# Performance work log

Measured on AMD Instinct MI355X. Metric: run time of the kernel, lower is better.

The kernel has to match this reference:

```python
import jax, jax.numpy as jnp
import numpy as np

N_NODES = 100000
N_EDGES = 600000
N_GRAPHS = 512
F_IN = 128
F_HID = 128
F_OUT = 128


def setup_inputs() -> dict:
    key = jax.random.key(0)
    ks = jax.random.split(key, 10)
    x = jax.random.normal(ks[0], (N_NODES, F_IN), dtype=jnp.float32)
    edge_index = jax.random.randint(ks[1], (2, N_EDGES), 0, N_NODES, dtype=jnp.int64)
    batch = jnp.sort(jax.random.randint(ks[2], (N_NODES,), 0, N_GRAPHS, dtype=jnp.int64))
    s1 = 1.0 / np.sqrt(F_IN)
    s2 = 1.0 / np.sqrt(F_HID)
    s3 = 1.0 / np.sqrt(F_OUT)
    W1 = jax.random.uniform(ks[3], (F_IN, F_HID), jnp.float32, -s1, s1)
    b1 = jnp.zeros((F_HID,), jnp.float32)
    W2 = jax.random.uniform(ks[4], (F_HID, F_OUT), jnp.float32, -s2, s2)
    b2 = jnp.zeros((F_OUT,), jnp.float32)
    Wlin = jax.random.uniform(ks[5], (F_OUT, 1), jnp.float32, -s3, s3)
    blin = jax.random.uniform(ks[6], (1,), jnp.float32, -s3, s3)
    return {"x": x, "edge_index": edge_index, "batch": batch,
            "W1": W1, "b1": b1, "W2": W2, "b2": b2, "Wlin": Wlin, "blin": blin}


def reference(x, edge_index, batch, W1, b1, W2, b2, Wlin, blin):
    N = x.shape[0]
    # GCN normalization with self-loops: D^{-1/2} (A + I) D^{-1/2}
    loop = jnp.arange(N, dtype=edge_index.dtype)
    src = jnp.concatenate([edge_index[0], loop])  # [E + N]
    dst = jnp.concatenate([edge_index[1], loop])
    deg = jax.ops.segment_sum(jnp.ones_like(dst, dtype=x.dtype), dst, num_segments=N)
    dis = jnp.where(deg > 0, jax.lax.rsqrt(jnp.maximum(deg, 1.0)), 0.0)  # deg^{-1/2}
    norm = (dis[src] * dis[dst])[:, None]  # [E+N, 1] edge weights

    def gcn_conv(h, W, b):
        hW = h @ W                                      # [N, d_out]
        msgs = norm * hW[src]                           # gather + scale
        agg = jax.ops.segment_sum(msgs, dst, num_segments=N)  # scatter-add
        return agg + b

    h = jax.nn.relu(gcn_conv(x, W1, b1))
    h = gcn_conv(h, W2, b2)

    # global_mean_pool over graph ids
    counts = jax.ops.segment_sum(jnp.ones((N,), x.dtype), batch, num_segments=N_GRAPHS)
    pooled = jax.ops.segment_sum(h, batch, num_segments=N_GRAPHS)
    pooled = pooled / jnp.maximum(counts, 1.0)[:, None]  # [N_GRAPHS, F_OUT]

    # dropout is identity in eval mode
    return pooled @ Wlin + blin  # [N_GRAPHS, 1]
```

## Files before the change

### kernel.cpp

```cpp
#include <hip/hip_runtime.h>

#define F 128

typedef __bf16 bf16x8 __attribute__((ext_vector_type(8)));
typedef float f32x4 __attribute__((ext_vector_type(4)));

__global__ __launch_bounds__(256) void k_prep(const float* __restrict__ W1, const float* __restrict__ W2,
                                              const float* __restrict__ Wlin, const float* __restrict__ b2,
                                              const float* __restrict__ blin, const int* __restrict__ batch,
                                              __bf16* __restrict__ Bswz, float* __restrict__ w2l,
                                              float* __restrict__ cconst, int* __restrict__ gstart,
                                              int* __restrict__ histg, float* __restrict__ deg,
                                              int N, int G, int bG) {
    int bid = blockIdx.x;
    int tid = threadIdx.x;
    if (bid < 64) {
        int o = bid * 256 + tid;
        int j = o & 7, lane = (o >> 3) & 63, tc = o >> 9;
        int t = tc >> 3, c = tc & 7;
        int k = t * 32 + (lane >> 4) * 8 + j;
        int n = c * 16 + (lane & 15);
        Bswz[o] = (__bf16)W1[k * F + n];
    } else if (bid == 64) {
        __shared__ float sh[F];
        if (tid < F) {
            float s = 0.0f;
            for (int j = 0; j < F; j += 4) {
                float4 w = *(const float4*)&W2[tid * F + j];
                float4 l = *(const float4*)&Wlin[j];
                s += w.x * l.x + w.y * l.y + w.z * l.z + w.w * l.w;
            }
            w2l[tid] = s;
            sh[tid] = b2[tid] * Wlin[tid];
        } else if (tid < F + 64) {
            histg[tid - F] = 0;
        }
        __syncthreads();
        if (tid == 0) {
            float c = blin[0];
            for (int j = 0; j < F; ++j) c += sh[j];
            *cconst = c;
        }
    } else if (bid < 65 + bG) {
        int g = (bid - 65) * 256 + tid;
        if (g < G) {
            int lo = 0, hi = N;
            while (lo < hi) { int mid = (lo + hi) >> 1; if (batch[mid] < g) lo = mid + 1; else hi = mid; }
            gstart[g] = lo;
            if (g == 0) gstart[G] = N;
        }
    } else {
        int i = (bid - 65 - bG) * 256 + tid;
        if (i < N) deg[i] = 1.0f;
    }
}

__global__ __launch_bounds__(256) void k_count(const int* __restrict__ dst, float* deg, int E) {
    int base = (blockIdx.x * 256 + threadIdx.x) * 4;
    if (base + 4 <= E) {
        int4 d = *(const int4*)(dst + base);
        unsafeAtomicAdd(&deg[d.x], 1.0f);
        unsafeAtomicAdd(&deg[d.y], 1.0f);
        unsafeAtomicAdd(&deg[d.z], 1.0f);
        unsafeAtomicAdd(&deg[d.w], 1.0f);
    } else {
        for (int i = base; i < E; ++i) unsafeAtomicAdd(&deg[dst[i]], 1.0f);
    }
}

__global__ __launch_bounds__(256) void k_scan1(const float* __restrict__ deg, int* __restrict__ pref,
                                               int* __restrict__ bsum, float* __restrict__ dis,
                                               int* __restrict__ histg, int N) {
    int t = threadIdx.x;
    __shared__ int lh[64];
    __shared__ int wtot[4];
    if (t < 64) lh[t] = 0;
    int base = blockIdx.x * 1024 + t * 4;
    int v[4]; int s = 0;
#pragma unroll
    for (int j = 0; j < 4; ++j) {
        int idx = base + j;
        float dv = (idx < N) ? deg[idx] : 1.0f;
        if (idx < N) dis[idx] = rsqrtf(dv);
        v[j] = (idx < N) ? ((int)dv - 1) : 0; s += v[j];
    }
    int lane = t & 63, w = t >> 6;
    int inc = s;
#pragma unroll
    for (int d = 1; d < 64; d <<= 1) { int o = __shfl_up(inc, d); if (lane >= d) inc += o; }
    if (lane == 63) wtot[w] = inc;
    __syncthreads();
#pragma unroll
    for (int j = 0; j < 4; ++j)
        if (base + j < N) atomicAdd(&lh[min(v[j], 63)], 1);
    int woff = 0;
#pragma unroll
    for (int i = 0; i < 4; ++i) if (i < w) woff += wtot[i];
    int run = woff + inc - s;
#pragma unroll
    for (int j = 0; j < 4; ++j) { int idx = base + j; if (idx < N) pref[idx] = run; run += v[j]; }
    if (t == 255) bsum[blockIdx.x] = woff + inc;
    __syncthreads();
    if (t < 64 && lh[t] > 0) atomicAdd(&histg[t], lh[t]);
}

__global__ __launch_bounds__(256) void k_scan3(int* __restrict__ pref, const int* __restrict__ bsum,
                                               int* __restrict__ cursor, const int* __restrict__ histg,
                                               int* __restrict__ bcur, int N, int E) {
    int t = threadIdx.x;
    int chunk = blockIdx.x >> 2;
    int partial = 0;
    for (int i = t; i < chunk; i += 256) partial += bsum[i];
    int lane = t & 63, w = t >> 6;
#pragma unroll
    for (int d = 1; d < 64; d <<= 1) partial += __shfl_xor(partial, d);
    __shared__ int ws4[4];
    if (lane == 0) ws4[w] = partial;
    __syncthreads();
    int off = ws4[0] + ws4[1] + ws4[2] + ws4[3];
    int i = blockIdx.x * 256 + t;
    if (i < N) {
        int v = pref[i] + off;
        pref[i] = v;
        cursor[i] = v;
    }
    if (i == 0) pref[N] = E;
    if (blockIdx.x == 0 && t < 64) {
        int h = histg[t];
        int inc2 = h;
#pragma unroll
        for (int d = 1; d < 64; d <<= 1) { int o = __shfl_up(inc2, d); if (t >= d) inc2 += o; }
        bcur[t] = inc2 - h;
    }
}

__global__ __launch_bounds__(256) void k_fill(const int* __restrict__ src, const int* __restrict__ dst,
                                              const float* __restrict__ deg, int* __restrict__ cursor,
                                              int* __restrict__ srcs, int* __restrict__ bcur,
                                              int* __restrict__ perm, int E, int N, int nbN) {
    int bid = blockIdx.x, tid = threadIdx.x;
    if (bid < nbN) {
        __shared__ int lcnt[64], lbase[64];
        if (tid < 64) lcnt[tid] = 0;
        __syncthreads();
        int n = bid * 256 + tid;
        int b = 0, r = 0;
        if (n < N) {
            b = min((int)deg[n] - 1, 63);
            r = atomicAdd(&lcnt[b], 1);
        }
        __syncthreads();
        if (tid < 64 && lcnt[tid] > 0) lbase[tid] = atomicAdd(&bcur[tid], lcnt[tid]);
        __syncthreads();
        if (n < N) perm[lbase[b] + r] = n;
    } else {
        int base = ((bid - nbN) * 256 + tid) * 4;
        if (base + 4 <= E) {
            int4 s4 = *(const int4*)(src + base);
            int4 d4 = *(const int4*)(dst + base);
            srcs[atomicAdd(&cursor[d4.x], 1)] = s4.x;
            srcs[atomicAdd(&cursor[d4.y], 1)] = s4.y;
            srcs[atomicAdd(&cursor[d4.z], 1)] = s4.z;
            srcs[atomicAdd(&cursor[d4.w], 1)] = s4.w;
        } else {
            for (int e = base; e < E; ++e) {
                srcs[atomicAdd(&cursor[dst[e]], 1)] = src[e];
            }
        }
    }
}

__global__ __launch_bounds__(256) void k_gemm_mfma(const float* __restrict__ X,
                                                   const __bf16* __restrict__ Bswz,
                                                   const float* __restrict__ dis,
                                                   __bf16* __restrict__ Yb, int N) {
    int lane = threadIdx.x & 63, wave = threadIdx.x >> 6;
    int quad = lane >> 4, m = lane & 15;
    int r0 = blockIdx.x * 128 + wave * 32;

    f32x4 acc[2][8];
#pragma unroll
    for (int rt = 0; rt < 2; ++rt)
#pragma unroll
        for (int c = 0; c < 8; ++c) acc[rt][c] = (f32x4)0.0f;

    int ra = r0 + m;      if (ra >= N) ra = N - 1;
    int rb = r0 + 16 + m; if (rb >= N) rb = N - 1;
    const float* pxa = &X[(size_t)ra * F + quad * 8];
    const float* pxb = &X[(size_t)rb * F + quad * 8];

    float4 a0 = *(const float4*)pxa, a1 = *(const float4*)(pxa + 4);
    float4 a2 = *(const float4*)pxb, a3 = *(const float4*)(pxb + 4);

#pragma unroll 1
    for (int t = 0; t < 4; ++t) {
        const __bf16* bp = Bswz + (size_t)t * 4096 + lane * 8;
        bf16x8 B[8];
#pragma unroll
        for (int c = 0; c < 8; ++c) B[c] = *(const bf16x8*)(bp + c * 512);

        float fa[8] = {a0.x, a0.y, a0.z, a0.w, a1.x, a1.y, a1.z, a1.w};
        float fb[8] = {a2.x, a2.y, a2.z, a2.w, a3.x, a3.y, a3.z, a3.w};
        bf16x8 ah0, al0, ah1, al1;
#pragma unroll
        for (int j = 0; j < 8; ++j) {
            __bf16 h0 = (__bf16)fa[j]; ah0[j] = h0; al0[j] = (__bf16)(fa[j] - (float)h0);
            __bf16 h1 = (__bf16)fb[j]; ah1[j] = h1; al1[j] = (__bf16)(fb[j] - (float)h1);
        }
        if (t < 3) {
            a0 = *(const float4*)(pxa + (t + 1) * 32);
            a1 = *(const float4*)(pxa + (t + 1) * 32 + 4);
            a2 = *(const float4*)(pxb + (t + 1) * 32);
            a3 = *(const float4*)(pxb + (t + 1) * 32 + 4);
        }
#pragma unroll
        for (int c = 0; c < 8; ++c) {
            acc[0][c] = __builtin_amdgcn_mfma_f32_16x16x32_bf16(ah0, B[c], acc[0][c], 0, 0, 0);
            acc[0][c] = __builtin_amdgcn_mfma_f32_16x16x32_bf16(al0, B[c], acc[0][c], 0, 0, 0);
            acc[1][c] = __builtin_amdgcn_mfma_f32_16x16x32_bf16(ah1, B[c], acc[1][c], 0, 0, 0);
            acc[1][c] = __builtin_amdgcn_mfma_f32_16x16x32_bf16(al1, B[c], acc[1][c], 0, 0, 0);
        }
    }

#pragma unroll
    for (int rt = 0; rt < 2; ++rt) {
        int rbase = r0 + rt * 16 + quad * 4;
#pragma unroll
        for (int r = 0; r < 4; ++r) {
            int row = rbase + r;
            if (row < N) {
                float dr = dis[row];
#pragma unroll
                for (int c = 0; c < 8; ++c)
                    Yb[(size_t)row * F + c * 16 + m] = (__bf16)(acc[rt][c][r] * dr);
            }
        }
    }
}

__global__ __launch_bounds__(256) void k_agg_z(const __bf16* __restrict__ hWb, const float* __restrict__ dis,
                                               const int* __restrict__ rowptr, const int* __restrict__ srcs,
                                               const int* __restrict__ perm,
                                               const float* __restrict__ bias, const float* __restrict__ w2l,
                                               float* __restrict__ zt, int N) {
    int idx = blockIdx.x * 32 + (threadIdx.x >> 3);
    if (idx >= N) return;
    int node = perm[idx];
    int lane = threadIdx.x & 7;
    float di = dis[node];
    float s[16];
    {
        const __bf16* pr = &hWb[(size_t)node * F + lane * 16];
        bf16x8 v0 = *(const bf16x8*)pr;
        bf16x8 v1 = *(const bf16x8*)(pr + 8);
#pragma unroll
        for (int j = 0; j < 8; ++j) { s[j] = (float)v0[j]; s[8 + j] = (float)v1[j]; }
    }
    int e0 = rowptr[node], e1 = rowptr[node + 1];
    int e = e0;
    for (; e + 4 <= e1; e += 4) {
        int i0 = srcs[e], i1 = srcs[e + 1], i2 = srcs[e + 2], i3 = srcs[e + 3];
        const __bf16* p0 = &hWb[(size_t)i0 * F + lane * 16];
        const __bf16* p1 = &hWb[(size_t)i1 * F + lane * 16];
        const __bf16* p2 = &hWb[(size_t)i2 * F + lane * 16];
        const __bf16* p3 = &hWb[(size_t)i3 * F + lane * 16];
        bf16x8 a0 = *(const bf16x8*)p0, b0 = *(const bf16x8*)(p0 + 8);
        bf16x8 a1 = *(const bf16x8*)p1, b1 = *(const bf16x8*)(p1 + 8);
        bf16x8 a2 = *(const bf16x8*)p2, b2 = *(const bf16x8*)(p2 + 8);
        bf16x8 a3 = *(const bf16x8*)p3, b3 = *(const bf16x8*)(p3 + 8);
#pragma unroll
        for (int j = 0; j < 8; ++j) {
            s[j]     += (float)a0[j] + (float)a1[j] + (float)a2[j] + (float)a3[j];
            s[8 + j] += (float)b0[j] + (float)b1[j] + (float)b2[j] + (float)b3[j];
        }
    }
    for (; e < e1; ++e) {
        const __bf16* pr = &hWb[(size_t)srcs[e] * F + lane * 16];
        bf16x8 v0 = *(const bf16x8*)pr;
        bf16x8 v1 = *(const bf16x8*)(pr + 8);
#pragma unroll
        for (int j = 0; j < 8; ++j) { s[j] += (float)v0[j]; s[8 + j] += (float)v1[j]; }
    }
    float p = 0.0f;
#pragma unroll
    for (int q = 0; q < 4; ++q) {
        float4 bb = *(const float4*)&bias[lane * 16 + q * 4];
        float4 ww = *(const float4*)&w2l[lane * 16 + q * 4];
        p += fmaxf(fmaf(di, s[q * 4 + 0], bb.x), 0.0f) * ww.x;
        p += fmaxf(fmaf(di, s[q * 4 + 1], bb.y), 0.0f) * ww.y;
        p += fmaxf(fmaf(di, s[q * 4 + 2], bb.z), 0.0f) * ww.z;
        p += fmaxf(fmaf(di, s[q * 4 + 3], bb.w), 0.0f) * ww.w;
    }
#pragma unroll
    for (int d = 1; d < 8; d <<= 1) p += __shfl_xor(p, d);
    if (lane == 0) zt[node] = di * p;
}

__global__ __launch_bounds__(256) void k_pool(const float* __restrict__ zt, const float* __restrict__ dis,
                                              const int* __restrict__ rowptr, const int* __restrict__ srcs,
                                              const int* __restrict__ gstart, const float* __restrict__ cconst,
                                              const float* __restrict__ blin, float* __restrict__ out, int G) {
    int g = blockIdx.x;
    int g0 = gstart[g], g1 = gstart[g + 1];
    float acc = 0.0f;
    for (int n = g0 + threadIdx.x; n < g1; n += 256) {
        float s = zt[n];
        int e0 = rowptr[n], e1 = rowptr[n + 1];
        int e = e0;
        for (; e + 4 <= e1; e += 4) {
            s += zt[srcs[e]] + zt[srcs[e + 1]] + zt[srcs[e + 2]] + zt[srcs[e + 3]];
        }
        for (; e < e1; ++e) s += zt[srcs[e]];
        acc += dis[n] * s;
    }
#pragma unroll
    for (int d = 1; d < 64; d <<= 1) acc += __shfl_xor(acc, d);
    __shared__ float ws4[4];
    if ((threadIdx.x & 63) == 0) ws4[threadIdx.x >> 6] = acc;
    __syncthreads();
    if (threadIdx.x == 0) {
        float sum = ws4[0] + ws4[1] + ws4[2] + ws4[3];
        int c = g1 - g0;
        out[g] = (c > 0) ? (sum / (float)c + cconst[0]) : blin[0];
    }
}


extern "C" void kernel_launch(void* const* d_in, const int* in_sizes, int n_in,
                              void* d_out, int out_size, void* d_ws, size_t ws_size,
                              hipStream_t stream) {
    const float* x    = (const float*)d_in[0];
    const int*   ei   = (const int*)d_in[1];
    const int*   batch= (const int*)d_in[2];
    const float* W1   = (const float*)d_in[3];
    const float* b1   = (const float*)d_in[4];
    const float* W2   = (const float*)d_in[5];
    const float* b2   = (const float*)d_in[6];
    const float* Wlin = (const float*)d_in[7];
    const float* blin = (const float*)d_in[8];
    float* out = (float*)d_out;

    const int N = in_sizes[2];
    const int E = in_sizes[1] / 2;
    const int G = out_size;
    const int* src = ei;
    const int* dst = ei + E;

    char* p = (char*)d_ws;
    auto take = [&](size_t bytes) { char* q = p; p += (bytes + 255) & ~(size_t)255; return q; };
    __bf16* hWb    = (__bf16*)take((size_t)N * F * 2);
    float*  ztbuf  = (float*)take((size_t)N * 4);
    float*  deg    = (float*)take((size_t)N * 4);
    float*  dis    = (float*)take((size_t)N * 4);
    int*    rowptr = (int*)  take((size_t)(N + 1) * 4);
    int*    cursor = (int*)  take((size_t)N * 4);
    int*    srcs   = (int*)  take((size_t)E * 4);
    int*    perm   = (int*)  take((size_t)N * 4);
    int*    bsum   = (int*)  take(4096);
    int*    histg  = (int*)  take(64 * 4);
    int*    bcur   = (int*)  take(64 * 4);
    int*    gstart = (int*)  take((size_t)(G + 1) * 4);
    float*  w2l    = (float*)take((size_t)F * 4);
    float*  cconst = (float*)take(256);
    __bf16* Bswz   = (__bf16*)take((size_t)F * F * 2);

    const int nbN  = (N + 255) / 256;
    const int nbE4 = (E + 1023) / 1024;
    const int nbS  = (N + 1023) / 1024;
    const int bG   = (G + 255) / 256;

    k_prep <<<65 + bG + nbN, 256, 0, stream>>>(W1, W2, Wlin, b2, blin, batch,
                                               Bswz, w2l, cconst, gstart, histg, deg, N, G, bG);
    k_count<<<nbE4, 256, 0, stream>>>(dst, deg, E);
    k_scan1<<<nbS, 256, 0, stream>>>(deg, rowptr, bsum, dis, histg, N);
    k_scan3<<<nbN, 256, 0, stream>>>(rowptr, bsum, cursor, histg, bcur, N, E);
    k_fill <<<nbN + nbE4, 256, 0, stream>>>(src, dst, deg, cursor, srcs, bcur, perm, E, N, nbN);

    k_gemm_mfma<<<(N + 127) / 128, 256, 0, stream>>>(x, Bswz, dis, hWb, N);
    k_agg_z<<<(N + 31) / 32, 256, 0, stream>>>(hWb, dis, rowptr, srcs, perm, b1, w2l, ztbuf, N);
    k_pool <<<G, 256, 0, stream>>>(ztbuf, dis, rowptr, srcs, gstart, cconst, blin, out, G);
}
```

Baseline: 222.8 us.

## Fuse CSR build into one cooperative kernel and parallelize pooling per node

Merges the degree count, two scan passes and CSR fill kernels into a single cooperative launch of persistent blocks separated by grid-wide syncs, which removes several kernel launch gaps. Pooling moves from one block per graph to one thread per degree-sorted node, adding each node's value into per-graph accumulators with atomics, followed by a small finalize kernel. The cooperative launch requires 1024 blocks to be co-resident, and grid syncs plus float atomics make the summation order nondeterministic.

```diff
diff --git a/kernel.cpp b/kernel.cpp
--- a/kernel.cpp
+++ b/kernel.cpp
@@ -1,4 +1,7 @@
 #include <hip/hip_runtime.h>
+#include <hip/hip_cooperative_groups.h>
+
+namespace cg = cooperative_groups;
 
 #define F 128
 
@@ -11,7 +14,7 @@
                                               __bf16* __restrict__ Bswz, float* __restrict__ w2l,
                                               float* __restrict__ cconst, int* __restrict__ gstart,
                                               int* __restrict__ histg, float* __restrict__ deg,
-                                              int N, int G, int bG) {
+                                              float* __restrict__ gacc, int N, int G, int bG) {
     int bid = blockIdx.x;
     int tid = threadIdx.x;
     if (bid < 64) {
@@ -47,6 +50,7 @@
             int lo = 0, hi = N;
             while (lo < hi) { int mid = (lo + hi) >> 1; if (batch[mid] < g) lo = mid + 1; else hi = mid; }
             gstart[g] = lo;
+            gacc[g] = 0.0f;
             if (g == 0) gstart[G] = N;
         }
     } else {
@@ -55,95 +59,96 @@
     }
 }
 
-__global__ __launch_bounds__(256) void k_count(const int* __restrict__ dst, float* deg, int E) {
-    int base = (blockIdx.x * 256 + threadIdx.x) * 4;
-    if (base + 4 <= E) {
-        int4 d = *(const int4*)(dst + base);
+__global__ __launch_bounds__(256, 4) void k_graph(const int* __restrict__ src, const int* __restrict__ dst,
+                                                  float* __restrict__ deg, int* __restrict__ pref,
+                                                  int* __restrict__ bsum, float* __restrict__ dis,
+                                                  int* __restrict__ histg, int* __restrict__ cursor,
+                                                  int* __restrict__ srcs, int* __restrict__ bcur,
+                                                  int* __restrict__ perm,
+                                                  int N, int E, int nbN, int nbS) {
+    cg::grid_group grid = cg::this_grid();
+    int tid = threadIdx.x;
+    int nthreads = gridDim.x * 256;
+    __shared__ int lh[64];
+    __shared__ int wtot[4];
+    __shared__ int ws4[4];
+    __shared__ int lcnt[64], lbase[64];
+
+    for (int i = blockIdx.x * 256 + tid; i < (E >> 2); i += nthreads) {
+        int4 d = *(const int4*)(dst + i * 4);
         unsafeAtomicAdd(&deg[d.x], 1.0f);
         unsafeAtomicAdd(&deg[d.y], 1.0f);
         unsafeAtomicAdd(&deg[d.z], 1.0f);
         unsafeAtomicAdd(&deg[d.w], 1.0f);
-    } else {
-        for (int i = base; i < E; ++i) unsafeAtomicAdd(&deg[dst[i]], 1.0f);
-    }
-}
-
-__global__ __launch_bounds__(256) void k_scan1(const float* __restrict__ deg, int* __restrict__ pref,
-                                               int* __restrict__ bsum, float* __restrict__ dis,
-                                               int* __restrict__ histg, int N) {
-    int t = threadIdx.x;
-    __shared__ int lh[64];
-    __shared__ int wtot[4];
-    if (t < 64) lh[t] = 0;
-    int base = blockIdx.x * 1024 + t * 4;
-    int v[4]; int s = 0;
-#pragma unroll
-    for (int j = 0; j < 4; ++j) {
-        int idx = base + j;
-        float dv = (idx < N) ? deg[idx] : 1.0f;
-        if (idx < N) dis[idx] = rsqrtf(dv);
-        v[j] = (idx < N) ? ((int)dv - 1) : 0; s += v[j];
-    }
-    int lane = t & 63, w = t >> 6;
-    int inc = s;
-#pragma unroll
-    for (int d = 1; d < 64; d <<= 1) { int o = __shfl_up(inc, d); if (lane >= d) inc += o; }
-    if (lane == 63) wtot[w] = inc;
-    __syncthreads();
-#pragma unroll
-    for (int j = 0; j < 4; ++j)
-        if (base + j < N) atomicAdd(&lh[min(v[j], 63)], 1);
-    int woff = 0;
-#pragma unroll
-    for (int i = 0; i < 4; ++i) if (i < w) woff += wtot[i];
-    int run = woff + inc - s;
-#pragma unroll
-    for (int j = 0; j < 4; ++j) { int idx = base + j; if (idx < N) pref[idx] = run; run += v[j]; }
-    if (t == 255) bsum[blockIdx.x] = woff + inc;
-    __syncthreads();
-    if (t < 64 && lh[t] > 0) atomicAdd(&histg[t], lh[t]);
-}
-
-__global__ __launch_bounds__(256) void k_scan3(int* __restrict__ pref, const int* __restrict__ bsum,
-                                               int* __restrict__ cursor, const int* __restrict__ histg,
-                                               int* __restrict__ bcur, int N, int E) {
-    int t = threadIdx.x;
-    int chunk = blockIdx.x >> 2;
-    int partial = 0;
-    for (int i = t; i < chunk; i += 256) partial += bsum[i];
-    int lane = t & 63, w = t >> 6;
-#pragma unroll
-    for (int d = 1; d < 64; d <<= 1) partial += __shfl_xor(partial, d);
-    __shared__ int ws4[4];
-    if (lane == 0) ws4[w] = partial;
-    __syncthreads();
-    int off = ws4[0] + ws4[1] + ws4[2] + ws4[3];
-    int i = blockIdx.x * 256 + t;
-    if (i < N) {
-        int v = pref[i] + off;
-        pref[i] = v;
-        cursor[i] = v;
-    }
-    if (i == 0) pref[N] = E;
-    if (blockIdx.x == 0 && t < 64) {
-        int h = histg[t];
+    }
+    if (blockIdx.x == 0 && tid < (E & 3))
+        unsafeAtomicAdd(&deg[dst[(E & ~3) + tid]], 1.0f);
+    grid.sync();
+
+    for (int vb = blockIdx.x; vb < nbS; vb += gridDim.x) {
+        if (tid < 64) lh[tid] = 0;
+        int base = vb * 1024 + tid * 4;
+        int v[4]; int s = 0;
+#pragma unroll
+        for (int j = 0; j < 4; ++j) {
+            int idx = base + j;
+            float dv = (idx < N) ? deg[idx] : 1.0f;
+            if (idx < N) dis[idx] = rsqrtf(dv);
+            v[j] = (idx < N) ? ((int)dv - 1) : 0; s += v[j];
+        }
+        int lane = tid & 63, w = tid >> 6;
+        int inc = s;
+#pragma unroll
+        for (int d = 1; d < 64; d <<= 1) { int o = __shfl_up(inc, d); if (lane >= d) inc += o; }
+        if (lane == 63) wtot[w] = inc;
+        __syncthreads();
+#pragma unroll
+        for (int j = 0; j < 4; ++j)
+            if (base + j < N) atomicAdd(&lh[min(v[j], 63)], 1);
+        int woff = 0;
+#pragma unroll
+        for (int i = 0; i < 4; ++i) if (i < w) woff += wtot[i];
+        int run = woff + inc - s;
+#pragma unroll
+        for (int j = 0; j < 4; ++j) { int idx = base + j; if (idx < N) pref[idx] = run; run += v[j]; }
+        if (tid == 255) bsum[vb] = woff + inc;
+        __syncthreads();
+        if (tid < 64 && lh[tid] > 0) atomicAdd(&histg[tid], lh[tid]);
+    }
+    grid.sync();
+
+    for (int vb = blockIdx.x; vb < nbN; vb += gridDim.x) {
+        int chunk = vb >> 2;
+        int partial = 0;
+        for (int i = tid; i < chunk; i += 256) partial += bsum[i];
+        int lane = tid & 63, w = tid >> 6;
+#pragma unroll
+        for (int d = 1; d < 64; d <<= 1) partial += __shfl_xor(partial, d);
+        if (lane == 0) ws4[w] = partial;
+        __syncthreads();
+        int off = ws4[0] + ws4[1] + ws4[2] + ws4[3];
+        int i2 = vb * 256 + tid;
+        if (i2 < N) {
+            int vv = pref[i2] + off;
+            pref[i2] = vv;
+            cursor[i2] = vv;
+        }
+        if (i2 == 0) pref[N] = E;
+        __syncthreads();
+    }
+    if (blockIdx.x == 0 && tid < 64) {
+        int h = histg[tid];
         int inc2 = h;
 #pragma unroll
-        for (int d = 1; d < 64; d <<= 1) { int o = __shfl_up(inc2, d); if (t >= d) inc2 += o; }
-        bcur[t] = inc2 - h;
-    }
-}
-
-__global__ __launch_bounds__(256) void k_fill(const int* __restrict__ src, const int* __restrict__ dst,
-                                              const float* __restrict__ deg, int* __restrict__ cursor,
-                                              int* __restrict__ srcs, int* __restrict__ bcur,
-                                              int* __restrict__ perm, int E, int N, int nbN) {
-    int bid = blockIdx.x, tid = threadIdx.x;
-    if (bid < nbN) {
-        __shared__ int lcnt[64], lbase[64];
+        for (int d = 1; d < 64; d <<= 1) { int o = __shfl_up(inc2, d); if (tid >= d) inc2 += o; }
+        bcur[tid] = inc2 - h;
+    }
+    grid.sync();
+
+    for (int vb = blockIdx.x; vb < nbN; vb += gridDim.x) {
         if (tid < 64) lcnt[tid] = 0;
         __syncthreads();
-        int n = bid * 256 + tid;
+        int n = vb * 256 + tid;
         int b = 0, r = 0;
         if (n < N) {
             b = min((int)deg[n] - 1, 63);
@@ -153,20 +158,19 @@
         if (tid < 64 && lcnt[tid] > 0) lbase[tid] = atomicAdd(&bcur[tid], lcnt[tid]);
         __syncthreads();
         if (n < N) perm[lbase[b] + r] = n;
-    } else {
-        int base = ((bid - nbN) * 256 + tid) * 4;
-        if (base + 4 <= E) {
-            int4 s4 = *(const int4*)(src + base);
-            int4 d4 = *(const int4*)(dst + base);
-            srcs[atomicAdd(&cursor[d4.x], 1)] = s4.x;
-            srcs[atomicAdd(&cursor[d4.y], 1)] = s4.y;
-            srcs[atomicAdd(&cursor[d4.z], 1)] = s4.z;
-            srcs[atomicAdd(&cursor[d4.w], 1)] = s4.w;
-        } else {
-            for (int e = base; e < E; ++e) {
-                srcs[atomicAdd(&cursor[dst[e]], 1)] = src[e];
-            }
-        }
+        __syncthreads();
+    }
+    for (int i = blockIdx.x * 256 + tid; i < (E >> 2); i += nthreads) {
+        int4 s4 = *(const int4*)(src + i * 4);
+        int4 d4 = *(const int4*)(dst + i * 4);
+        srcs[atomicAdd(&cursor[d4.x], 1)] = s4.x;
+        srcs[atomicAdd(&cursor[d4.y], 1)] = s4.y;
+        srcs[atomicAdd(&cursor[d4.z], 1)] = s4.z;
+        srcs[atomicAdd(&cursor[d4.w], 1)] = s4.w;
+    }
+    if (blockIdx.x == 0 && tid < (E & 3)) {
+        int e = (E & ~3) + tid;
+        srcs[atomicAdd(&cursor[dst[e]], 1)] = src[e];
     }
 }
 
@@ -298,30 +302,28 @@
 
 __global__ __launch_bounds__(256) void k_pool(const float* __restrict__ zt, const float* __restrict__ dis,
                                               const int* __restrict__ rowptr, const int* __restrict__ srcs,
-                                              const int* __restrict__ gstart, const float* __restrict__ cconst,
-                                              const float* __restrict__ blin, float* __restrict__ out, int G) {
-    int g = blockIdx.x;
-    int g0 = gstart[g], g1 = gstart[g + 1];
-    float acc = 0.0f;
-    for (int n = g0 + threadIdx.x; n < g1; n += 256) {
-        float s = zt[n];
-        int e0 = rowptr[n], e1 = rowptr[n + 1];
-        int e = e0;
-        for (; e + 4 <= e1; e += 4) {
-            s += zt[srcs[e]] + zt[srcs[e + 1]] + zt[srcs[e + 2]] + zt[srcs[e + 3]];
-        }
-        for (; e < e1; ++e) s += zt[srcs[e]];
-        acc += dis[n] * s;
-    }
-#pragma unroll
-    for (int d = 1; d < 64; d <<= 1) acc += __shfl_xor(acc, d);
-    __shared__ float ws4[4];
-    if ((threadIdx.x & 63) == 0) ws4[threadIdx.x >> 6] = acc;
-    __syncthreads();
-    if (threadIdx.x == 0) {
-        float sum = ws4[0] + ws4[1] + ws4[2] + ws4[3];
-        int c = g1 - g0;
-        out[g] = (c > 0) ? (sum / (float)c + cconst[0]) : blin[0];
+                                              const int* __restrict__ perm, const int* __restrict__ batch,
+                                              float* __restrict__ gacc, int N) {
+    int idx = blockIdx.x * 256 + threadIdx.x;
+    if (idx >= N) return;
+    int n = perm[idx];
+    float s = zt[n];
+    int e0 = rowptr[n], e1 = rowptr[n + 1];
+    int e = e0;
+    for (; e + 4 <= e1; e += 4) {
+        s += zt[srcs[e]] + zt[srcs[e + 1]] + zt[srcs[e + 2]] + zt[srcs[e + 3]];
+    }
+    for (; e < e1; ++e) s += zt[srcs[e]];
+    unsafeAtomicAdd(&gacc[batch[n]], dis[n] * s);
+}
+
+__global__ __launch_bounds__(256) void k_final(const float* __restrict__ gacc, const int* __restrict__ gstart,
+                                               const float* __restrict__ cconst, const float* __restrict__ blin,
+                                               float* __restrict__ out, int G) {
+    int g = blockIdx.x * 256 + threadIdx.x;
+    if (g < G) {
+        int c = gstart[g + 1] - gstart[g];
+        out[g] = (c > 0) ? (gacc[g] / (float)c + cconst[0]) : blin[0];
     }
 }
 
@@ -360,23 +362,29 @@
     int*    histg  = (int*)  take(64 * 4);
     int*    bcur   = (int*)  take(64 * 4);
     int*    gstart = (int*)  take((size_t)(G + 1) * 4);
+    float*  gacc   = (float*)take((size_t)G * 4);
     float*  w2l    = (float*)take((size_t)F * 4);
     float*  cconst = (float*)take(256);
     __bf16* Bswz   = (__bf16*)take((size_t)F * F * 2);
 
     const int nbN  = (N + 255) / 256;
-    const int nbE4 = (E + 1023) / 1024;
     const int nbS  = (N + 1023) / 1024;
     const int bG   = (G + 255) / 256;
 
-    k_prep <<<65 + bG + nbN, 256, 0, stream>>>(W1, W2, Wlin, b2, blin, batch,
-                                               Bswz, w2l, cconst, gstart, histg, deg, N, G, bG);
-    k_count<<<nbE4, 256, 0, stream>>>(dst, deg, E);
-    k_scan1<<<nbS, 256, 0, stream>>>(deg, rowptr, bsum, dis, histg, N);
-    k_scan3<<<nbN, 256, 0, stream>>>(rowptr, bsum, cursor, histg, bcur, N, E);
-    k_fill <<<nbN + nbE4, 256, 0, stream>>>(src, dst, deg, cursor, srcs, bcur, perm, E, N, nbN);
+    k_prep<<<65 + bG + nbN, 256, 0, stream>>>(W1, W2, Wlin, b2, blin, batch,
+                                              Bswz, w2l, cconst, gstart, histg, deg, gacc, N, G, bG);
+
+    {
+        const int* srcp = src; const int* dstp = dst;
+        int Nv = N, Ev = E, nbNv = nbN, nbSv = nbS;
+        void* kargs[] = { (void*)&srcp, (void*)&dstp, (void*)&deg, (void*)&rowptr, (void*)&bsum,
+                          (void*)&dis, (void*)&histg, (void*)&cursor, (void*)&srcs, (void*)&bcur,
+                          (void*)&perm, (void*)&Nv, (void*)&Ev, (void*)&nbNv, (void*)&nbSv };
+        hipLaunchCooperativeKernel((void*)k_graph, dim3(1024), dim3(256), kargs, 0, stream);
+    }
 
     k_gemm_mfma<<<(N + 127) / 128, 256, 0, stream>>>(x, Bswz, dis, hWb, N);
     k_agg_z<<<(N + 31) / 32, 256, 0, stream>>>(hWb, dis, rowptr, srcs, perm, b1, w2l, ztbuf, N);
-    k_pool <<<G, 256, 0, stream>>>(ztbuf, dis, rowptr, srcs, gstart, cconst, blin, out, G);
-}
+    k_pool<<<nbN, 256, 0, stream>>>(ztbuf, dis, rowptr, srcs, perm, batch, gacc, N);
+    k_final<<<bG, 256, 0, stream>>>(gacc, gstart, cconst, blin, out, G);
+}
```

Result: slower. 582.6 us (+161.5%).

## Parallelize mean pooling per node with atomics instead of per-graph blocks

Applied to the files above, without the earlier changes.

The pooling step changes from one block per graph, each looping over that graph's nodes, to one thread per node in degree-sorted order. Each thread gathers its neighbour contributions and atomically adds the result into a per-graph accumulator. A small final kernel then divides by the node counts and adds the constant. This is meant to spread the work evenly across the GPU and fix the load imbalance between graphs, at the cost of float atomic contention on 512 accumulators, an extra launch, and a non-deterministic summation order.

```diff
diff --git a/kernel.cpp b/kernel.cpp
--- a/kernel.cpp
+++ b/kernel.cpp
@@ -11,7 +11,7 @@
                                               __bf16* __restrict__ Bswz, float* __restrict__ w2l,
                                               float* __restrict__ cconst, int* __restrict__ gstart,
                                               int* __restrict__ histg, float* __restrict__ deg,
-                                              int N, int G, int bG) {
+                                              float* __restrict__ gacc, int N, int G, int bG) {
     int bid = blockIdx.x;
     int tid = threadIdx.x;
     if (bid < 64) {
@@ -47,6 +47,7 @@
             int lo = 0, hi = N;
             while (lo < hi) { int mid = (lo + hi) >> 1; if (batch[mid] < g) lo = mid + 1; else hi = mid; }
             gstart[g] = lo;
+            gacc[g] = 0.0f;
             if (g == 0) gstart[G] = N;
         }
     } else {
@@ -298,30 +299,28 @@
 
 __global__ __launch_bounds__(256) void k_pool(const float* __restrict__ zt, const float* __restrict__ dis,
                                               const int* __restrict__ rowptr, const int* __restrict__ srcs,
-                                              const int* __restrict__ gstart, const float* __restrict__ cconst,
-                                              const float* __restrict__ blin, float* __restrict__ out, int G) {
-    int g = blockIdx.x;
-    int g0 = gstart[g], g1 = gstart[g + 1];
-    float acc = 0.0f;
-    for (int n = g0 + threadIdx.x; n < g1; n += 256) {
-        float s = zt[n];
-        int e0 = rowptr[n], e1 = rowptr[n + 1];
-        int e = e0;
-        for (; e + 4 <= e1; e += 4) {
-            s += zt[srcs[e]] + zt[srcs[e + 1]] + zt[srcs[e + 2]] + zt[srcs[e + 3]];
-        }
-        for (; e < e1; ++e) s += zt[srcs[e]];
-        acc += dis[n] * s;
-    }
-#pragma unroll
-    for (int d = 1; d < 64; d <<= 1) acc += __shfl_xor(acc, d);
-    __shared__ float ws4[4];
-    if ((threadIdx.x & 63) == 0) ws4[threadIdx.x >> 6] = acc;
-    __syncthreads();
-    if (threadIdx.x == 0) {
-        float sum = ws4[0] + ws4[1] + ws4[2] + ws4[3];
-        int c = g1 - g0;
-        out[g] = (c > 0) ? (sum / (float)c + cconst[0]) : blin[0];
+                                              const int* __restrict__ perm, const int* __restrict__ batch,
+                                              float* __restrict__ gacc, int N) {
+    int idx = blockIdx.x * 256 + threadIdx.x;
+    if (idx >= N) return;
+    int n = perm[idx];
+    float s = zt[n];
+    int e0 = rowptr[n], e1 = rowptr[n + 1];
+    int e = e0;
+    for (; e + 4 <= e1; e += 4) {
+        s += zt[srcs[e]] + zt[srcs[e + 1]] + zt[srcs[e + 2]] + zt[srcs[e + 3]];
+    }
+    for (; e < e1; ++e) s += zt[srcs[e]];
+    unsafeAtomicAdd(&gacc[batch[n]], dis[n] * s);
+}
+
+__global__ __launch_bounds__(256) void k_final(const float* __restrict__ gacc, const int* __restrict__ gstart,
+                                               const float* __restrict__ cconst, const float* __restrict__ blin,
+                                               float* __restrict__ out, int G) {
+    int g = blockIdx.x * 256 + threadIdx.x;
+    if (g < G) {
+        int c = gstart[g + 1] - gstart[g];
+        out[g] = (c > 0) ? (gacc[g] / (float)c + cconst[0]) : blin[0];
     }
 }
 
@@ -360,6 +359,7 @@
     int*    histg  = (int*)  take(64 * 4);
     int*    bcur   = (int*)  take(64 * 4);
     int*    gstart = (int*)  take((size_t)(G + 1) * 4);
+    float*  gacc   = (float*)take((size_t)G * 4);
     float*  w2l    = (float*)take((size_t)F * 4);
     float*  cconst = (float*)take(256);
     __bf16* Bswz   = (__bf16*)take((size_t)F * F * 2);
@@ -370,7 +370,7 @@
     const int bG   = (G + 255) / 256;
 
     k_prep <<<65 + bG + nbN, 256, 0, stream>>>(W1, W2, Wlin, b2, blin, batch,
-                                               Bswz, w2l, cconst, gstart, histg, deg, N, G, bG);
+                                               Bswz, w2l, cconst, gstart, histg, deg, gacc, N, G, bG);
     k_count<<<nbE4, 256, 0, stream>>>(dst, deg, E);
     k_scan1<<<nbS, 256, 0, stream>>>(deg, rowptr, bsum, dis, histg, N);
     k_scan3<<<nbN, 256, 0, stream>>>(rowptr, bsum, cursor, histg, bcur, N, E);
@@ -378,5 +378,6 @@
 
     k_gemm_mfma<<<(N + 127) / 128, 256, 0, stream>>>(x, Bswz, dis, hWb, N);
     k_agg_z<<<(N + 31) / 32, 256, 0, stream>>>(hWb, dis, rowptr, srcs, perm, b1, w2l, ztbuf, N);
-    k_pool <<<G, 256, 0, stream>>>(ztbuf, dis, rowptr, srcs, gstart, cconst, blin, out, G);
-}
+    k_pool <<<nbN, 256, 0, stream>>>(ztbuf, dis, rowptr, srcs, perm, batch, gacc, N);
+    k_final<<<bG, 256, 0, stream>>>(gacc, gstart, cconst, blin, out, G);
+}
```

Result: slower. 292.6 us (+31.3%).
